# Performance work log

Hardware: AMD Instinct MI355X
Metric: run time of the kernel (lower is better)

## Reference

```python
import jax, jax.numpy as jnp
import numpy as np

S, HID, H, KV, D = 2048, 3584, 16, 8, 256
WINDOW = 1024
SOFTCAP = 50.0
SCALING = 256 ** (-0.5)  # query_pre_attn_scalar ** -0.5
EPS = 1e-6
ROPE_THETA = 10000.0


def _rope_tables(seq_len, dim, theta):
    inv_freq = 1.0 / (theta ** (np.arange(0, dim, 2, dtype=np.float32) / dim))
    t = np.arange(seq_len, dtype=np.float32)
    freqs = np.outer(t, inv_freq)            # [S, D/2]
    emb = np.concatenate([freqs, freqs], -1)  # [S, D]
    return jnp.asarray(np.cos(emb)), jnp.asarray(np.sin(emb))


def setup_inputs() -> dict:
    key = jax.random.key(0)
    ks = jax.random.split(key, 3)
    hidden_states = jax.random.normal(ks[0], (S, HID), jnp.float32)
    w_qkv = jax.random.normal(ks[1], (HID, (H + 2 * KV) * D), jnp.float32) * (HID ** -0.5)
    w_o = jax.random.normal(ks[2], (H * D, HID), jnp.float32) * ((H * D) ** -0.5)
    q_norm_w = jnp.zeros((D,), jnp.float32)  # gemma norm stores weight as (1 + w)
    k_norm_w = jnp.zeros((D,), jnp.float32)
    cos, sin = _rope_tables(S, D, ROPE_THETA)
    return {"hidden_states": hidden_states, "w_qkv": w_qkv, "w_o": w_o,
            "q_norm_w": q_norm_w, "k_norm_w": k_norm_w, "cos": cos, "sin": sin}


def _rms_norm(x, w):
    # gemma-style: fp32 norm, scale by (1 + w); x: [S, h, D]
    xf = x.astype(jnp.float32)
    var = jnp.mean(xf * xf, axis=-1, keepdims=True)
    return (xf * jax.lax.rsqrt(var + EPS) * (1.0 + w)).astype(x.dtype)


def _rotate_half(x):
    x1, x2 = jnp.split(x, 2, axis=-1)
    return jnp.concatenate([-x2, x1], axis=-1)


def _apply_rope(x, cos, sin):
    # x: [S, h, D]; cos/sin: [S, D]
    c = cos[:, None, :]
    s = sin[:, None, :]
    return x * c + _rotate_half(x) * s


def reference(hidden_states, w_qkv, w_o, q_norm_w, k_norm_w, cos, sin):
    qkv = hidden_states @ w_qkv                      # [S, (H+2KV)*D]
    q = qkv[:, : H * D].reshape(S, H, D)
    k = qkv[:, H * D: (H + KV) * D].reshape(S, KV, D)
    v = qkv[:, (H + KV) * D:].reshape(S, KV, D)

    q = _rms_norm(q, q_norm_w)                       # gemma3 q_norm
    k = _rms_norm(k, k_norm_w)                       # gemma3 k_norm
    q = _apply_rope(q, cos, sin)
    k = _apply_rope(k, cos, sin)

    # GQA: expand KV heads to H
    rep = H // KV
    k = jnp.repeat(k, rep, axis=1)                   # [S, H, D]
    v = jnp.repeat(v, rep, axis=1)

    scores = jnp.einsum('shd,thd->hst', q, k) * SCALING  # [H, S, S]
    scores = SOFTCAP * jnp.tanh(scores / SOFTCAP)        # logit softcapping

    i = jnp.arange(S)[:, None]
    j = jnp.arange(S)[None, :]
    allowed = (j <= i) & ((i - j) < WINDOW)              # causal + sliding window
    scores = jnp.where(allowed[None], scores, jnp.float32(-1e30))

    attn = jax.nn.softmax(scores, axis=-1)
    out = jnp.einsum('hst,thd->shd', attn, v).reshape(S, H * D)
    return out @ w_o                                     # [S, HID]
```

## Files before the change

kernel.cpp:

```cpp
#include <hip/hip_runtime.h>
#include <hip/hip_bf16.h>
#include <math.h>

typedef __attribute__((ext_vector_type(8))) short short8;
typedef __attribute__((ext_vector_type(4))) float floatx4;
typedef unsigned short u16;

typedef __attribute__((address_space(1))) const void* gas_ptr;
typedef __attribute__((address_space(3))) void* las_ptr;

__device__ __forceinline__ float bf2f(u16 h) {
  union { unsigned u; float f; } v; v.u = ((unsigned)h) << 16; return v.f;
}
__device__ __forceinline__ u16 f2bf(float f) {
  union { float f; unsigned u; } v; v.f = f;
  unsigned r = v.u + 0x7FFFu + ((v.u >> 16) & 1u);
  return (u16)(r >> 16);
}
__device__ __forceinline__ float ldf_dyn(const void* p, size_t i, bool f32) {
  return f32 ? ((const float*)p)[i] : bf2f(((const u16*)p)[i]);
}
__device__ __forceinline__ short8 load8_dyn(const void* p, size_t idx, bool f32) {
  if (f32) {
    const float* f = (const float*)p;
    float4 a = *(const float4*)(f + idx);
    float4 b = *(const float4*)(f + idx + 4);
    short8 r;
    r[0] = (short)f2bf(a.x); r[1] = (short)f2bf(a.y);
    r[2] = (short)f2bf(a.z); r[3] = (short)f2bf(a.w);
    r[4] = (short)f2bf(b.x); r[5] = (short)f2bf(b.y);
    r[6] = (short)f2bf(b.z); r[7] = (short)f2bf(b.w);
    return r;
  }
  return *(const short8*)((const u16*)p + idx);
}
__device__ __forceinline__ void gl_lds16(const u16* g, u16* l) {
  __builtin_amdgcn_global_load_lds((gas_ptr)g, (las_ptr)l, 16, 0, 0);
}

__global__ void probe_dtype_kernel(const void* hidden, int* flag) {
  __shared__ int cnt;
  if (threadIdx.x == 0) cnt = 0;
  __syncthreads();
  const u16* h = (const u16*)hidden;
  int local = 0;
  for (int i = threadIdx.x; i < 8192; i += 256) {
    u16 u = h[i];
    int e = (u >> 7) & 0xFF;
    if ((e >= 64 && e <= 160) || (u & 0x7FFF) == 0) local++;
  }
  atomicAdd(&cnt, local);
  __syncthreads();
  if (threadIdx.x == 0) *flag = (cnt < 7700) ? 1 : 0;
}

__global__ __launch_bounds__(256) void convert_dyn_kernel(
    const void* __restrict__ src, u16* __restrict__ dst, size_t n,
    const int* __restrict__ flagp)
{
  if (*flagp == 0) return;
  size_t i = ((size_t)blockIdx.x * 256 + threadIdx.x) * 8;
  if (i < n) *(short8*)(dst + i) = load8_dyn(src, i, true);
}

__global__ __launch_bounds__(256) void transpose_dyn_kernel(
    const void* __restrict__ src, u16* __restrict__ dst, int R, int C,
    const int* __restrict__ flagp)
{
  const bool f32 = (*flagp != 0);
  const int c0 = blockIdx.x * 64, r0 = blockIdx.y * 64;
  __shared__ __attribute__((aligned(16))) u16 T[64][72];
  const int tid = threadIdx.x;
#pragma unroll
  for (int i = 0; i < 2; i++) {
    int t = tid + i * 256;
    int r = t >> 3, cc = (t & 7) << 3;
    *(short8*)(&T[r][cc]) = load8_dyn(src, (size_t)(r0 + r) * C + c0 + cc, f32);
  }
  __syncthreads();
#pragma unroll
  for (int i = 0; i < 2; i++) {
    int t = tid + i * 256;
    int cr = t >> 3, rc = (t & 7) << 3;
    __attribute__((aligned(16))) u16 tmp[8];
#pragma unroll
    for (int j = 0; j < 8; j++) tmp[j] = T[rc + j][cr];
    *(short8*)(dst + (size_t)(c0 + cr) * R + r0 + rc) = *(const short8*)tmp;
  }
}

#define BAR() __builtin_amdgcn_s_barrier()
#define SCB() __builtin_amdgcn_sched_barrier(0)
#define LGKM0() do { asm volatile("s_waitcnt lgkmcnt(0)" ::: "memory"); SCB(); } while (0)
#define LGKMC(n) do { asm volatile("s_waitcnt lgkmcnt(" #n ")" ::: "memory"); SCB(); } while (0)
#define VMW(n) do { asm volatile("s_waitcnt vmcnt(" #n ")" ::: "memory"); SCB(); } while (0)
#define PRIO1() __builtin_amdgcn_s_setprio(1)
#define PRIO0() do { __builtin_amdgcn_s_setprio(0); SCB(); } while (0)

#define STG_AU(s, u, t) \
  gl_lds16(pa + (size_t)((u) * 64) * K + (size_t)(t) * 64, \
           ldsw + (s) * 32768 + (u) * 4096)
#define STG_BU(s, u, t) \
  gl_lds16(pb + (size_t)((u) * 64) * K + (size_t)(t) * 64, \
           ldsw + (s) * 32768 + 16384 + (u) * 4096)

#define RD_FA(s, miH) do { \
  _Pragma("unroll") \
  for (int m2 = 0; m2 < 4; m2++) { \
    const u16* _r = LDS + (s) * 32768 + wm * 8192 + (miH) * 4096 + m2 * 1024 + lane15 * 64; \
    fa[m2][0] = *(const short8*)(_r + colA0); \
    fa[m2][1] = *(const short8*)(_r + colA1); \
  } \
} while (0)
#define RD_FB(s, niH) do { \
  _Pragma("unroll") \
  for (int n2 = 0; n2 < 2; n2++) { \
    const u16* _r = LDS + (s) * 32768 + 16384 + wn * 4096 + (niH) * 2048 + n2 * 1024 + lane15 * 64; \
    fb[niH][n2][0] = *(const short8*)(_r + colA0); \
    fb[niH][n2][1] = *(const short8*)(_r + colA1); \
  } \
} while (0)
#define RD_FA1(s, miH, m2v) do { \
  const u16* _r = LDS + (s) * 32768 + wm * 8192 + (miH) * 4096 + (m2v) * 1024 + lane15 * 64; \
  fa[m2v][0] = *(const short8*)(_r + colA0); \
  fa[m2v][1] = *(const short8*)(_r + colA1); \
} while (0)
#define RD_FB1(s, niH, n2v) do { \
  const u16* _r = LDS + (s) * 32768 + 16384 + wn * 4096 + (niH) * 2048 + (n2v) * 1024 + lane15 * 64; \
  fb[niH][n2v][0] = *(const short8*)(_r + colA0); \
  fb[niH][n2v][1] = *(const short8*)(_r + colA1); \
} while (0)

#define MFMA_M2(m2v, miH, niH) do { \
  _Pragma("unroll") \
  for (int n2 = 0; n2 < 2; n2++) { \
    acc[(miH) * 4 + (m2v)][(niH) * 2 + n2] = __builtin_amdgcn_mfma_f32_16x16x32_bf16( \
        fa[m2v][0], fb[niH][n2][0], acc[(miH) * 4 + (m2v)][(niH) * 2 + n2], 0, 0, 0); \
    acc[(miH) * 4 + (m2v)][(niH) * 2 + n2] = __builtin_amdgcn_mfma_f32_16x16x32_bf16( \
        fa[m2v][1], fb[niH][n2][1], acc[(miH) * 4 + (m2v)][(niH) * 2 + n2], 0, 0, 0); \
  } \
} while (0)
#define MFMA_N2(n2v, miH, niH) do { \
  _Pragma("unroll") \
  for (int m2 = 0; m2 < 4; m2++) { \
    acc[(miH) * 4 + m2][(niH) * 2 + (n2v)] = __builtin_amdgcn_mfma_f32_16x16x32_bf16( \
        fa[m2][0], fb[niH][n2v][0], acc[(miH) * 4 + m2][(niH) * 2 + (n2v)], 0, 0, 0); \
    acc[(miH) * 4 + m2][(niH) * 2 + (n2v)] = __builtin_amdgcn_mfma_f32_16x16x32_bf16( \
        fa[m2][1], fb[niH][n2v][1], acc[(miH) * 4 + m2][(niH) * 2 + (n2v)], 0, 0, 0); \
  } \
} while (0)
#define MFMA_Q(miH, niH) do { \
  PRIO1(); \
  _Pragma("unroll") \
  for (int m2 = 0; m2 < 4; m2++) \
    _Pragma("unroll") \
    for (int n2 = 0; n2 < 2; n2++) { \
      acc[(miH) * 4 + m2][(niH) * 2 + n2] = __builtin_amdgcn_mfma_f32_16x16x32_bf16( \
          fa[m2][0], fb[niH][n2][0], acc[(miH) * 4 + m2][(niH) * 2 + n2], 0, 0, 0); \
      acc[(miH) * 4 + m2][(niH) * 2 + n2] = __builtin_amdgcn_mfma_f32_16x16x32_bf16( \
          fa[m2][1], fb[niH][n2][1], acc[(miH) * 4 + m2][(niH) * 2 + n2], 0, 0, 0); \
    } \
  PRIO0(); \
} while (0)

__global__ __launch_bounds__(512, 2) void gemm8p_kernel(
    const void* __restrict__ Araw, const u16* __restrict__ Ahb,
    const u16* __restrict__ BT, u16* __restrict__ C,
    int M, int N, int K, const int* __restrict__ flagp)
{
  __shared__ __attribute__((aligned(16))) u16 LDS[65536];
  const int tid = threadIdx.x;
  const int wave = tid >> 6, lane = tid & 63;
  const int lane15 = lane & 15, quad = lane >> 4;
  const int wm = wave >> 2, wn = wave & 3;
  const int m0 = blockIdx.y * 256, n0 = blockIdx.x * 256;

  const u16* Abase = (*flagp != 0) ? Ahb : (const u16*)Araw;

  const int rloc = wave * 8 + (lane >> 3);
  const int sxor = lane >> 3;
  const int csw = ((lane & 7) ^ sxor) * 8;
  const u16* pa = Abase + (size_t)(m0 + rloc) * K + csw;
  const u16* pb = BT + (size_t)(n0 + rloc) * K + csw;
  u16* ldsw = LDS + wave * 512;

  const int swz = lane15 & 7;
  const int colA0 = (quad ^ swz) * 8;
  const int colA1 = ((4 + quad) ^ swz) * 8;

  floatx4 acc[8][4];
#pragma unroll
  for (int i = 0; i < 8; i++)
#pragma unroll
    for (int j = 0; j < 4; j++) acc[i][j] = (floatx4){0.f, 0.f, 0.f, 0.f};
  short8 fa[4][2], fb[2][2][2];

  const int NT = K >> 6, NI = NT >> 1;

  STG_AU(0, 0, 0); STG_AU(0, 2, 0);
  STG_BU(0, 0, 0); STG_BU(0, 1, 0);
  STG_BU(0, 2, 0); STG_BU(0, 3, 0);
  STG_AU(0, 1, 0); STG_AU(0, 3, 0);
  STG_AU(1, 0, 1); STG_AU(1, 2, 1);
  STG_BU(1, 0, 1); STG_BU(1, 1, 1);
  STG_BU(1, 2, 1); STG_BU(1, 3, 1);
  VMW(8);
  BAR();

  for (int i = 0; i < NI - 1; i++) {
    const int t1 = 2 * i + 1, t2 = 2 * i + 2, t3 = 2 * i + 3;
    RD_FB(0, 0); SCB();
    RD_FA1(0, 0, 0); SCB(); RD_FA1(0, 0, 1); SCB();
    RD_FA1(0, 0, 2); SCB(); RD_FA1(0, 0, 3); SCB();
    STG_AU(1, 1, t1); STG_AU(1, 3, t1);
    BAR(); PRIO1();
    LGKMC(6); MFMA_M2(0, 0, 0);
    LGKMC(4); MFMA_M2(1, 0, 0);
    LGKMC(2); MFMA_M2(2, 0, 0);
    LGKM0();  MFMA_M2(3, 0, 0);
    PRIO0(); BAR();
    RD_FB1(0, 1, 0); SCB(); RD_FB1(0, 1, 1); SCB();
    STG_AU(0, 0, t2); STG_AU(0, 2, t2);
    BAR(); PRIO1();
    LGKMC(2); MFMA_N2(0, 0, 1);
    LGKM0();  MFMA_N2(1, 0, 1);
    PRIO0(); VMW(10); BAR();
    RD_FA1(0, 1, 0); SCB(); RD_FA1(0, 1, 1); SCB();
    RD_FA1(0, 1, 2); SCB(); RD_FA1(0, 1, 3); SCB();
    STG_BU(0, 0, t2); STG_BU(0, 1, t2);
    BAR(); PRIO1();
    LGKMC(6); MFMA_M2(0, 1, 1);
    LGKMC(4); MFMA_M2(1, 1, 1);
    LGKMC(2); MFMA_M2(2, 1, 1);
    LGKM0();  MFMA_M2(3, 1, 1);
    PRIO0(); BAR();
    STG_BU(0, 2, t2); STG_BU(0, 3, t2);
    BAR(); MFMA_Q(1, 0); VMW(8); BAR();
    RD_FB(1, 0); SCB();
    RD_FA1(1, 0, 0); SCB(); RD_FA1(1, 0, 1); SCB();
    RD_FA1(1, 0, 2); SCB(); RD_FA1(1, 0, 3); SCB();
    STG_AU(0, 1, t2); STG_AU(0, 3, t2);
    BAR(); PRIO1();
    LGKMC(6); MFMA_M2(0, 0, 0);
    LGKMC(4); MFMA_M2(1, 0, 0);
    LGKMC(2); MFMA_M2(2, 0, 0);
    LGKM0();  MFMA_M2(3, 0, 0);
    PRIO0(); BAR();
    RD_FB1(1, 1, 0); SCB(); RD_FB1(1, 1, 1); SCB();
    STG_AU(1, 0, t3); STG_AU(1, 2, t3);
    BAR(); PRIO1();
    LGKMC(2); MFMA_N2(0, 0, 1);
    LGKM0();  MFMA_N2(1, 0, 1);
    PRIO0(); VMW(10); BAR();
    RD_FA1(1, 1, 0); SCB(); RD_FA1(1, 1, 1); SCB();
    RD_FA1(1, 1, 2); SCB(); RD_FA1(1, 1, 3); SCB();
    STG_BU(1, 0, t3); STG_BU(1, 1, t3);
    BAR(); PRIO1();
    LGKMC(6); MFMA_M2(0, 1, 1);
    LGKMC(4); MFMA_M2(1, 1, 1);
    LGKMC(2); MFMA_M2(2, 1, 1);
    LGKM0();  MFMA_M2(3, 1, 1);
    PRIO0(); BAR();
    STG_BU(1, 2, t3); STG_BU(1, 3, t3);
    BAR(); MFMA_Q(1, 0); VMW(8); BAR();
  }

  {
    const int tL = NT - 1;
    RD_FA(0, 0); RD_FB(0, 0);
    STG_AU(1, 1, tL); STG_AU(1, 3, tL);
    BAR(); LGKM0(); MFMA_Q(0, 0); BAR();
    RD_FB(0, 1);
    BAR(); LGKM0(); MFMA_Q(0, 1); VMW(8); BAR();
    RD_FA(0, 1);
    BAR(); LGKM0(); MFMA_Q(1, 1); BAR();
    BAR(); MFMA_Q(1, 0); VMW(2); BAR();
    RD_FA(1, 0); RD_FB(1, 0);
    BAR(); LGKM0(); MFMA_Q(0, 0); BAR();
    RD_FB(1, 1);
    BAR(); LGKM0(); MFMA_Q(0, 1); VMW(0); BAR();
    RD_FA(1, 1);
    BAR(); LGKM0(); MFMA_Q(1, 1); BAR();
    BAR(); MFMA_Q(1, 0);
  }

#pragma unroll
  for (int mi = 0; mi < 8; mi++)
#pragma unroll
    for (int rr = 0; rr < 4; rr++) {
      int m = m0 + wm * 128 + mi * 16 + quad * 4 + rr;
      u16* crow = C + (size_t)m * N + n0 + wn * 64;
#pragma unroll
      for (int ni = 0; ni < 4; ni++) crow[ni * 16 + lane15] = f2bf(acc[mi][ni][rr]);
    }
}

#define NSTG_A(s, u, t) \
  gl_lds16(pa + (size_t)((u) * 64) * K + (size_t)(t) * 64, \
           ldsw + (s) * 24576 + (u) * 4096)
#define NSTG_B(s, u, t) \
  gl_lds16(pb + (size_t)((u) * 64) * K + (size_t)(t) * 64, \
           ldsw + (s) * 24576 + 8192 + (u) * 4096)

#define NRD_FA(s, miH) do { \
  _Pragma("unroll") \
  for (int m2 = 0; m2 < 2; m2++) { \
    const u16* _r = LDS + (s) * 24576 + wm * 4096 + (miH) * 2048 + m2 * 1024 + lane15 * 64; \
    fa[m2][0] = *(const short8*)(_r + colA0); \
    fa[m2][1] = *(const short8*)(_r + colA1); \
  } \
} while (0)
#define NRD_FB(s, niH) do { \
  _Pragma("unroll") \
  for (int n2 = 0; n2 < 2; n2++) { \
    const u16* _r = LDS + (s) * 24576 + 8192 + wn * 4096 + (niH) * 2048 + n2 * 1024 + lane15 * 64; \
    fb[niH][n2][0] = *(const short8*)(_r + colA0); \
    fb[niH][n2][1] = *(const short8*)(_r + colA1); \
  } \
} while (0)
#define NMFMA_Q(miH, niH) do { \
  PRIO1(); \
  _Pragma("unroll") \
  for (int m2 = 0; m2 < 2; m2++) \
    _Pragma("unroll") \
    for (int n2 = 0; n2 < 2; n2++) { \
      acc[(miH) * 2 + m2][(niH) * 2 + n2] = __builtin_amdgcn_mfma_f32_16x16x32_bf16( \
          fa[m2][0], fb[niH][n2][0], acc[(miH) * 2 + m2][(niH) * 2 + n2], 0, 0, 0); \
      acc[(miH) * 2 + m2][(niH) * 2 + n2] = __builtin_amdgcn_mfma_f32_16x16x32_bf16( \
          fa[m2][1], fb[niH][n2][1], acc[(miH) * 2 + m2][(niH) * 2 + n2], 0, 0, 0); \
    } \
  PRIO0(); \
} while (0)

__global__ __launch_bounds__(512, 2) void gemm8pn_kernel(
    const u16* __restrict__ A, const u16* __restrict__ BT, void* __restrict__ C,
    int M, int N, int K, const int* __restrict__ flagp, int cdyn)
{
  __shared__ __attribute__((aligned(16))) u16 LDS[49152];
  const int tid = threadIdx.x;
  const int wave = tid >> 6, lane = tid & 63;
  const int lane15 = lane & 15, quad = lane >> 4;
  const int wm = wave >> 2, wn = wave & 3;
  const int m0 = blockIdx.y * 128, n0 = blockIdx.x * 256;

  const int rloc = wave * 8 + (lane >> 3);
  const int sxor = lane >> 3;
  const int csw = ((lane & 7) ^ sxor) * 8;
  const u16* pa = A + (size_t)(m0 + rloc) * K + csw;
  const u16* pb = BT + (size_t)(n0 + rloc) * K + csw;
  u16* ldsw = LDS + wave * 512;

  const int swz = lane15 & 7;
  const int colA0 = (quad ^ swz) * 8;
  const int colA1 = ((4 + quad) ^ swz) * 8;

  floatx4 acc[4][4];
#pragma unroll
  for (int i = 0; i < 4; i++)
#pragma unroll
    for (int j = 0; j < 4; j++) acc[i][j] = (floatx4){0.f, 0.f, 0.f, 0.f};
  short8 fa[2][2], fb[2][2][2];

  const int NT = K >> 6, NI = NT >> 1;

  NSTG_B(0, 0, 0); NSTG_B(0, 1, 0); NSTG_B(0, 2, 0); NSTG_B(0, 3, 0);
  NSTG_A(0, 0, 0); NSTG_A(0, 1, 0);
  NSTG_B(1, 0, 1); NSTG_B(1, 1, 1); NSTG_B(1, 2, 1); NSTG_B(1, 3, 1);
  NSTG_A(1, 0, 1); NSTG_A(1, 1, 1);
  VMW(6);
  BAR();

  for (int i = 0; i < NI - 1; i++) {
    const int t2 = 2 * i + 2, t3 = 2 * i + 3;
    NRD_FA(0, 0); NRD_FB(0, 0);
    BAR(); LGKM0(); NMFMA_Q(0, 0); BAR();
    NRD_FB(0, 1);
    BAR(); LGKM0(); NMFMA_Q(0, 1); BAR();
    NRD_FA(0, 1);
    NSTG_B(0, 0, t2); NSTG_B(0, 1, t2);
    BAR(); LGKM0(); NMFMA_Q(1, 1); BAR();
    NSTG_B(0, 2, t2); NSTG_B(0, 3, t2); NSTG_A(0, 0, t2); NSTG_A(0, 1, t2);
    BAR(); NMFMA_Q(1, 0); VMW(6); BAR();
    NRD_FA(1, 0); NRD_FB(1, 0);
    BAR(); LGKM0(); NMFMA_Q(0, 0); BAR();
    NRD_FB(1, 1);
    BAR(); LGKM0(); NMFMA_Q(0, 1); BAR();
    NRD_FA(1, 1);
    NSTG_B(1, 0, t3); NSTG_B(1, 1, t3);
    BAR(); LGKM0(); NMFMA_Q(1, 1); BAR();
    NSTG_B(1, 2, t3); NSTG_B(1, 3, t3); NSTG_A(1, 0, t3); NSTG_A(1, 1, t3);
    BAR(); NMFMA_Q(1, 0); VMW(6); BAR();
  }

  {
    NRD_FA(0, 0); NRD_FB(0, 0);
    BAR(); LGKM0(); NMFMA_Q(0, 0); BAR();
    NRD_FB(0, 1);
    BAR(); LGKM0(); NMFMA_Q(0, 1); BAR();
    NRD_FA(0, 1);
    BAR(); LGKM0(); NMFMA_Q(1, 1); BAR();
    BAR(); NMFMA_Q(1, 0); VMW(0); BAR();
    NRD_FA(1, 0); NRD_FB(1, 0);
    BAR(); LGKM0(); NMFMA_Q(0, 0); BAR();
    NRD_FB(1, 1);
    BAR(); LGKM0(); NMFMA_Q(0, 1); BAR();
    NRD_FA(1, 1);
    BAR(); LGKM0(); NMFMA_Q(1, 1); BAR();
    NMFMA_Q(1, 0);
  }

  const bool cf32 = cdyn && (*flagp != 0);
  if (cf32) {
    float* Cf = (float*)C;
#pragma unroll
    for (int mi = 0; mi < 4; mi++)
#pragma unroll
      for (int rr = 0; rr < 4; rr++) {
        int m = m0 + wm * 64 + mi * 16 + quad * 4 + rr;
        float* crow = Cf + (size_t)m * N + n0 + wn * 64;
#pragma unroll
        for (int ni = 0; ni < 4; ni++) crow[ni * 16 + lane15] = acc[mi][ni][rr];
      }
  } else {
    u16* Cb = (u16*)C;
#pragma unroll
    for (int mi = 0; mi < 4; mi++)
#pragma unroll
      for (int rr = 0; rr < 4; rr++) {
        int m = m0 + wm * 64 + mi * 16 + quad * 4 + rr;
        u16* crow = Cb + (size_t)m * N + n0 + wn * 64;
#pragma unroll
        for (int ni = 0; ni < 4; ni++) crow[ni * 16 + lane15] = f2bf(acc[mi][ni][rr]);
      }
  }
}

__global__ __launch_bounds__(256) void normrope_kernel(
    u16* __restrict__ qkv, const void* __restrict__ qw,
    const void* __restrict__ kw, const void* __restrict__ cosb,
    const void* __restrict__ sinb, const int* __restrict__ flagp)
{
  const bool f32 = (*flagp != 0);
  const int s = blockIdx.x;
  const int wave = threadIdx.x >> 6, lane = threadIdx.x & 63;
  const int hh = blockIdx.y * 4 + wave;
  const int col = (hh < 16) ? hh * 256 : 4096 + (hh - 16) * 256;
  const void* w = (hh < 16) ? qw : kw;
  u16* row = qkv + (size_t)s * 8192 + col;

  float x[4];
#pragma unroll
  for (int j = 0; j < 4; j++) x[j] = bf2f(row[lane + j * 64]);

  float ss = x[0] * x[0] + x[1] * x[1] + x[2] * x[2] + x[3] * x[3];
#pragma unroll
  for (int off = 32; off > 0; off >>= 1) ss += __shfl_xor(ss, off);
  float inv = rsqrtf(ss * (1.0f / 256.0f) + 1e-6f);

  float y[4];
#pragma unroll
  for (int j = 0; j < 4; j++)
    y[j] = x[j] * inv * (1.0f + ldf_dyn(w, lane + j * 64, f32));
  float rot[4] = {-y[2], -y[3], y[0], y[1]};
#pragma unroll
  for (int j = 0; j < 4; j++) {
    int d = lane + j * 64;
    float c = ldf_dyn(cosb, (size_t)s * 256 + d, f32);
    float sn = ldf_dyn(sinb, (size_t)s * 256 + d, f32);
    row[d] = f2bf(y[j] * c + rot[j] * sn);
  }
}

__global__ __launch_bounds__(256) void vtrans_kernel(
    const u16* __restrict__ qkv, u16* __restrict__ vT)
{
  const int s0 = blockIdx.x * 64, d0 = blockIdx.y * 64, kv = blockIdx.z;
  __shared__ __attribute__((aligned(16))) u16 T[64][72];
  const int tid = threadIdx.x;
#pragma unroll
  for (int i = 0; i < 2; i++) {
    int c = tid + i * 256;
    int r = c >> 3, dc = (c & 7) << 3;
    *(short8*)(&T[r][dc]) =
        *(const short8*)(qkv + (size_t)(s0 + r) * 8192 + 6144 + kv * 256 + d0 + dc);
  }
  __syncthreads();
#pragma unroll
  for (int i = 0; i < 2; i++) {
    int c = tid + i * 256;
    int dr = c >> 3, sc = (c & 7) << 3;
    __attribute__((aligned(16))) u16 tmp[8];
#pragma unroll
    for (int j = 0; j < 8; j++) tmp[j] = T[sc + j][dr];
    *(short8*)(vT + (size_t)kv * 524288 + (size_t)(d0 + dr) * 2048 + s0 + sc) =
        *(const short8*)tmp;
  }
}

__global__ __launch_bounds__(512) void attn_kernel(
    const u16* __restrict__ qkv, const u16* __restrict__ vT,
    u16* __restrict__ aout)
{
  const int h = blockIdx.y, kvh = h >> 1;
  const int q0 = blockIdx.x * 128;
  const int tid = threadIdx.x;
  const int wave = tid >> 6, lane = tid & 63;
  const int lane15 = lane & 15, quad = lane >> 4;

  __shared__ __attribute__((aligned(16))) u16 Ks[64 * 264];
  __shared__ __attribute__((aligned(16))) u16 Vs[256 * 72];
  __shared__ __attribute__((aligned(16))) u16 Ps[8][16 * 72];

  short8 aq[8];
  const u16* qrow = qkv + (size_t)(q0 + wave * 16 + lane15) * 8192 + h * 256;
#pragma unroll
  for (int kt = 0; kt < 8; kt++)
    aq[kt] = *(const short8*)(qrow + kt * 32 + quad * 8);

  floatx4 zero = {0.0f, 0.0f, 0.0f, 0.0f};
  floatx4 accO[16];
#pragma unroll
  for (int i = 0; i < 16; i++) accO[i] = zero;
  float lR[4] = {0.0f, 0.0f, 0.0f, 0.0f};

  const int iRow = q0 + wave * 16 + quad * 4;
  const int kb_lo = (q0 >= 1023) ? ((q0 - 1023) >> 6) : 0;
  const int kb_hi = (q0 + 127) >> 6;

  for (int kb = kb_lo; kb <= kb_hi; kb++) {
    const int t0 = kb << 6;
#pragma unroll
    for (int i = 0; i < 4; i++) {
      int c = tid + i * 512;
      int r = c >> 5, dc = (c & 31) << 3;
      *(short8*)(&Ks[r * 264 + dc]) =
          *(const short8*)(qkv + (size_t)(t0 + r) * 8192 + 4096 + kvh * 256 + dc);
    }
#pragma unroll
    for (int i = 0; i < 4; i++) {
      int c = tid + i * 512;
      int dr = c >> 3, tc = (c & 7) << 3;
      *(short8*)(&Vs[dr * 72 + tc]) =
          *(const short8*)(vT + (size_t)kvh * 524288 + (size_t)dr * 2048 + t0 + tc);
    }
    __syncthreads();

    const int relHi = q0 + 16 * wave + 15 - t0;
    const int relLo = q0 + 16 * wave - 1023 - t0;
    const int niHiR = relHi >> 4;
    const int niHi = (niHiR > 3) ? 3 : niHiR;
    int niLo = relLo >> 4; if (niLo < 0) niLo = 0;
    const int ktHiR = relHi >> 5;
    const int ktHi = (ktHiR > 1) ? 1 : ktHiR;
    int ktLo = relLo >> 5; if (ktLo < 0) ktLo = 0;

    float pv[4][4];
#pragma unroll
    for (int ni = 0; ni < 4; ni++) {
      if (ni < niLo || ni > niHi) {
        pv[ni][0] = pv[ni][1] = pv[ni][2] = pv[ni][3] = 0.0f;
        continue;
      }
      floatx4 sAcc = zero;
#pragma unroll
      for (int kt = 0; kt < 8; kt++) {
        short8 bk = *(const short8*)(&Ks[(ni * 16 + lane15) * 264 + kt * 32 + quad * 8]);
        sAcc = __builtin_amdgcn_mfma_f32_16x16x32_bf16(aq[kt], bk, sAcc, 0, 0, 0);
      }
#pragma unroll
      for (int r = 0; r < 4; r++) {
        float x = sAcc[r] * 0.00125f;
        float ax = __builtin_fabsf(x);
        float e2 = __expf(ax + ax);
        float t = 1.0f - 2.0f * __builtin_amdgcn_rcpf(e2 + 1.0f);
        float sv = copysignf(t, x) * 50.0f;
        int i_ = iRow + r;
        int j_ = t0 + ni * 16 + lane15;
        bool ok = (j_ <= i_) && (i_ - j_ < 1024);
        pv[ni][r] = ok ? __expf(sv) : 0.0f;
      }
    }
#pragma unroll
    for (int r = 0; r < 4; r++)
      lR[r] += pv[0][r] + pv[1][r] + pv[2][r] + pv[3][r];

#pragma unroll
    for (int ni = 0; ni < 4; ni++)
#pragma unroll
      for (int r = 0; r < 4; r++)
        Ps[wave][(quad * 4 + r) * 72 + ni * 16 + lane15] = f2bf(pv[ni][r]);
    __syncthreads();

#pragma unroll
    for (int ktile = 0; ktile < 2; ktile++) {
      if (ktile < ktLo || ktile > ktHi) continue;
      short8 ap = *(const short8*)(&Ps[wave][lane15 * 72 + ktile * 32 + quad * 8]);
#pragma unroll
      for (int ni = 0; ni < 16; ni++) {
        short8 bv = *(const short8*)(&Vs[(ni * 16 + lane15) * 72 + ktile * 32 + quad * 8]);
        accO[ni] = __builtin_amdgcn_mfma_f32_16x16x32_bf16(ap, bv, accO[ni], 0, 0, 0);
      }
    }
    __syncthreads();
  }

#pragma unroll
  for (int r = 0; r < 4; r++) {
    float l = lR[r];
    l += __shfl_xor(l, 1);
    l += __shfl_xor(l, 2);
    l += __shfl_xor(l, 4);
    l += __shfl_xor(l, 8);
    float invl = 1.0f / l;
    u16* orow = aout + (size_t)(q0 + wave * 16 + quad * 4 + r) * 4096 + h * 256;
#pragma unroll
    for (int ni = 0; ni < 16; ni++)
      orow[ni * 16 + lane15] = f2bf(accO[ni][r] * invl);
  }
}

extern "C" void kernel_launch(void* const* d_in, const int* in_sizes, int n_in,
                              void* d_out, int out_size, void* d_ws, size_t ws_size,
                              hipStream_t stream)
{
  const void* hidden = d_in[0];
  const void* w_qkv  = d_in[1];
  const void* w_o    = d_in[2];
  const void* q_w    = d_in[3];
  const void* k_w    = d_in[4];
  const void* cosb   = d_in[5];
  const void* sinb   = d_in[6];

  char* ws = (char*)d_ws;
  int* flag = (int*)ws;                                   ws += 256;
  u16* qkv  = (u16*)ws;  ws += (size_t)2048 * 8192 * 2;
  u16* vT   = (u16*)ws;  ws += (size_t)8 * 256 * 2048 * 2;
  u16* aout = (u16*)ws;  ws += (size_t)2048 * 4096 * 2;
  u16* hb   = (u16*)ws;  ws += (size_t)2048 * 3584 * 2;
  u16* wT   = (u16*)ws;

  probe_dtype_kernel<<<1, 256, 0, stream>>>(hidden, flag);
  convert_dyn_kernel<<<3584, 256, 0, stream>>>(hidden, hb, (size_t)2048 * 3584, flag);
  transpose_dyn_kernel<<<dim3(128, 56), 256, 0, stream>>>(w_qkv, wT, 3584, 8192, flag);
  gemm8p_kernel<<<dim3(32, 8), 512, 0, stream>>>(hidden, hb, wT, qkv, 2048, 8192, 3584, flag);
  normrope_kernel<<<dim3(2048, 6), 256, 0, stream>>>(qkv, q_w, k_w, cosb, sinb, flag);
  transpose_dyn_kernel<<<dim3(56, 64), 256, 0, stream>>>(w_o, wT, 4096, 3584, flag);
  vtrans_kernel<<<dim3(32, 4, 8), 256, 0, stream>>>(qkv, vT);
  attn_kernel<<<dim3(16, 16), 512, 0, stream>>>(qkv, vT, aout);
  gemm8pn_kernel<<<dim3(14, 16), 512, 0, stream>>>(aout, wT, d_out, 2048, 3584, 4096, flag, 1);
}
```

Measured before the change: 517.8 us.

## Double-buffer K/V tiles in attention with register prefetch of next block

Attention kernel now keeps two LDS buffers for K and V tiles. It loads the next KV block's global data into registers at the start of each iteration and writes them to the alternate buffer after the PV MMAs, which removes one barrier per iteration. The goal is to hide global load latency behind the QK, softmax and PV compute. In exchange it doubles K/V LDS usage (about 140KB total with Ps) and adds 8 short8 registers per thread, which may limit occupancy.

Result: no change. 519.8 us (+0.4%).

```diff
diff --git a/kernel.cpp b/kernel.cpp
--- a/kernel.cpp
+++ b/kernel.cpp
@@ -507,8 +507,8 @@
   const int wave = tid >> 6, lane = tid & 63;
   const int lane15 = lane & 15, quad = lane >> 4;
 
-  __shared__ __attribute__((aligned(16))) u16 Ks[64 * 264];
-  __shared__ __attribute__((aligned(16))) u16 Vs[256 * 72];
+  __shared__ __attribute__((aligned(16))) u16 Ks[2][64 * 264];
+  __shared__ __attribute__((aligned(16))) u16 Vs[2][256 * 72];
   __shared__ __attribute__((aligned(16))) u16 Ps[8][16 * 72];
 
   short8 aq[8];
@@ -527,23 +527,48 @@
   const int kb_lo = (q0 >= 1023) ? ((q0 - 1023) >> 6) : 0;
   const int kb_hi = (q0 + 127) >> 6;
 
-  for (int kb = kb_lo; kb <= kb_hi; kb++) {
-    const int t0 = kb << 6;
+  {
+    const int t0 = kb_lo << 6;
 #pragma unroll
     for (int i = 0; i < 4; i++) {
       int c = tid + i * 512;
       int r = c >> 5, dc = (c & 31) << 3;
-      *(short8*)(&Ks[r * 264 + dc]) =
+      *(short8*)(&Ks[0][r * 264 + dc]) =
           *(const short8*)(qkv + (size_t)(t0 + r) * 8192 + 4096 + kvh * 256 + dc);
     }
 #pragma unroll
     for (int i = 0; i < 4; i++) {
       int c = tid + i * 512;
       int dr = c >> 3, tc = (c & 7) << 3;
-      *(short8*)(&Vs[dr * 72 + tc]) =
+      *(short8*)(&Vs[0][dr * 72 + tc]) =
           *(const short8*)(vT + (size_t)kvh * 524288 + (size_t)dr * 2048 + t0 + tc);
     }
-    __syncthreads();
+  }
+  __syncthreads();
+
+  int cur = 0;
+  for (int kb = kb_lo; kb <= kb_hi; kb++) {
+    const int t0 = kb << 6;
+    const int nxt = cur ^ 1;
+    const bool pre = (kb < kb_hi);
+
+    short8 kr[4], vr[4];
+    if (pre) {
+      const int t0n = t0 + 64;
+#pragma unroll
+      for (int i = 0; i < 4; i++) {
+        int c = tid + i * 512;
+        int r = c >> 5, dc = (c & 31) << 3;
+        kr[i] = *(const short8*)(qkv + (size_t)(t0n + r) * 8192 + 4096 + kvh * 256 + dc);
+      }
+#pragma unroll
+      for (int i = 0; i < 4; i++) {
+        int c = tid + i * 512;
+        int dr = c >> 3, tc = (c & 7) << 3;
+        vr[i] = *(const short8*)(vT + (size_t)kvh * 524288 + (size_t)dr * 2048 + t0n + tc);
+      }
+    }
+    SCB();
 
     const int relHi = q0 + 16 * wave + 15 - t0;
     const int relLo = q0 + 16 * wave - 1023 - t0;
@@ -564,7 +589,7 @@
       floatx4 sAcc = zero;
 #pragma unroll
       for (int kt = 0; kt < 8; kt++) {
-        short8 bk = *(const short8*)(&Ks[(ni * 16 + lane15) * 264 + kt * 32 + quad * 8]);
+        short8 bk = *(const short8*)(&Ks[cur][(ni * 16 + lane15) * 264 + kt * 32 + quad * 8]);
         sAcc = __builtin_amdgcn_mfma_f32_16x16x32_bf16(aq[kt], bk, sAcc, 0, 0, 0);
       }
 #pragma unroll
@@ -597,11 +622,27 @@
       short8 ap = *(const short8*)(&Ps[wave][lane15 * 72 + ktile * 32 + quad * 8]);
 #pragma unroll
       for (int ni = 0; ni < 16; ni++) {
-        short8 bv = *(const short8*)(&Vs[(ni * 16 + lane15) * 72 + ktile * 32 + quad * 8]);
+        short8 bv = *(const short8*)(&Vs[cur][(ni * 16 + lane15) * 72 + ktile * 32 + quad * 8]);
         accO[ni] = __builtin_amdgcn_mfma_f32_16x16x32_bf16(ap, bv, accO[ni], 0, 0, 0);
+      }
+    }
+
+    if (pre) {
+#pragma unroll
+      for (int i = 0; i < 4; i++) {
+        int c = tid + i * 512;
+        int r = c >> 5, dc = (c & 31) << 3;
+        *(short8*)(&Ks[nxt][r * 264 + dc]) = kr[i];
+      }
+#pragma unroll
+      for (int i = 0; i < 4; i++) {
+        int c = tid + i * 512;
+        int dr = c >> 3, tc = (c & 7) << 3;
+        *(short8*)(&Vs[nxt][dr * 72 + tc]) = vr[i];
       }
     }
     __syncthreads();
+    cur = nxt;
   }
 
 #pragma unroll
```
